# Optimization experiments

Measured on AMD Instinct MI355X. Metric: run time of the kernel, lower is better.

## Reference

```python
import jax, jax.numpy as jnp
import numpy as np

E = 64          # num experts
IN = 512        # input_size
OUT = 512       # output_size
N = 131072      # total tokens = sum(expert_size)
CAP = 3072      # static per-expert capacity (>= max expert_size)


def _make_expert_sizes():
    # uneven but deterministic sizes summing to N, all <= CAP
    rng = np.random.default_rng(0)
    sizes = np.full(E, N // E, dtype=np.int32)
    d = rng.integers(0, 513, size=E // 2).astype(np.int32)
    sizes[0::2] += d
    sizes[1::2] -= d
    assert sizes.sum() == N and sizes.max() <= CAP and sizes.min() > 0
    return jnp.asarray(sizes, dtype=jnp.int32)


def setup_inputs() -> dict:
    key = jax.random.key(0)
    k1, k2 = jax.random.split(key)
    inputs = jax.random.normal(k1, (N, IN), dtype=jnp.float32)
    # matches nn.init.uniform_(weight, -1/in, 1/in)
    weight = jax.random.uniform(k2, (E, IN, OUT), dtype=jnp.float32,
                                minval=-1.0 / IN, maxval=1.0 / IN)
    expert_size = _make_expert_sizes()
    return {"inputs": inputs, "expert_size": expert_size, "weight": weight}


def reference(inputs, expert_size, weight):
    # Grouped GEMM: tokens are pre-sorted by expert; segment e is
    # inputs[offset[e]:offset[e]+expert_size[e]] @ weight[e].
    cap_ids = jnp.arange(CAP, dtype=jnp.int32)                # [CAP]
    offsets = jnp.cumsum(expert_size) - expert_size           # [E]
    idx = offsets[:, None] + cap_ids[None, :]                 # [E, CAP]
    valid = cap_ids[None, :] < expert_size[:, None]           # [E, CAP]
    idx = jnp.where(valid, idx, N)                            # invalid -> OOB (dropped)
    # gather tokens into padded per-expert blocks; invalid slots -> 0
    x = jnp.take(inputs, idx, axis=0, mode='fill', fill_value=0.0)  # [E, CAP, IN]
    h = jnp.einsum('eci,eio->eco', x, weight)                 # [E, CAP, OUT]
    out = jnp.zeros((N, OUT), dtype=inputs.dtype)
    out = out.at[idx.reshape(-1)].add(h.reshape(-1, OUT), mode='drop')
    return out
```

## Files before the change

### kernel.cpp

```cpp
#include <hip/hip_runtime.h>
#include <hip/hip_bf16.h>

#define E_NUM 64
#define IN_SZ 512
#define OUT_SZ 512
#define N_TOK 131072
#define CAP 3072

#define BM 256
#define BN 256
#define BK 64
#define THREADS 512
#define RT_MAX 12
#define CT_NUM 2
#define JT 8
#define NWG (E_NUM * RT_MAX * CT_NUM)

typedef __attribute__((ext_vector_type(8))) short short8;
typedef __attribute__((ext_vector_type(4))) float f32x4;

__device__ inline unsigned short f2bf(float f) {
    unsigned int u = __float_as_uint(f);
    unsigned int r = (u + 0x7FFF + ((u >> 16) & 1)) >> 16;
    return (unsigned short)r;
}

__device__ inline unsigned int cvtpk(float a, float b) {
    unsigned int r;
    asm("v_cvt_pk_bf16_f32 %0, %1, %2" : "=v"(r) : "v"(a), "v"(b));
    return r;
}

#define GLOAD_LDS16(g, l)                                                     \
    __builtin_amdgcn_global_load_lds(                                         \
        (const __attribute__((address_space(1))) void*)(g),                   \
        (__attribute__((address_space(3))) void*)(l), 16, 0, 0)

__global__ void offsets_kernel(const int* __restrict__ sizes, int* __restrict__ offs) {
    int e = threadIdx.x;
    int s = 0;
    for (int i = 0; i < e; ++i) s += sizes[i];
    offs[e] = s;
}

__global__ __launch_bounds__(256) void prep_wt(const float* __restrict__ W,
                                               unsigned short* __restrict__ WT) {
    __shared__ float t[32][33];
    int k0 = blockIdx.x * 32, n0 = blockIdx.y * 32, e = blockIdx.z;
    const float* We = W + (size_t)e * IN_SZ * OUT_SZ;
    int tid = threadIdx.x;
    int r = tid >> 3, c4 = (tid & 7) * 4;
    float4 v = *(const float4*)(We + (size_t)(k0 + r) * OUT_SZ + n0 + c4);
    t[r][c4 + 0] = v.x; t[r][c4 + 1] = v.y; t[r][c4 + 2] = v.z; t[r][c4 + 3] = v.w;
    __syncthreads();
    ushort4 o;
    o.x = f2bf(t[c4 + 0][r]);
    o.y = f2bf(t[c4 + 1][r]);
    o.z = f2bf(t[c4 + 2][r]);
    o.w = f2bf(t[c4 + 3][r]);
    unsigned short* O = WT + (size_t)e * IN_SZ * OUT_SZ + (size_t)(n0 + r) * IN_SZ + k0 + c4;
    *(ushort4*)O = o;
}

__global__ __launch_bounds__(THREADS, 2) void gemm_moe(
    const float* __restrict__ A, const int* __restrict__ sizes,
    const unsigned short* __restrict__ WT, const int* __restrict__ offs,
    float* __restrict__ out)
{
    int b0 = blockIdx.x;
    int wg = (b0 & 7) * (NWG / 8) + (b0 >> 3);
    int ct = wg & (CT_NUM - 1);
    int rt = (wg >> 1) % RT_MAX;
    int e  = wg / (RT_MAX * CT_NUM);

    int size_e = sizes[e];
    int rows0 = rt * BM;
    if (rows0 >= size_e) return;
    int off_e = offs[e];
    int rows_rem = size_e - rows0;
    int maxr = (rows_rem < BM ? rows_rem : BM) - 1;

    __shared__ unsigned short lsA[2][BM * BK];
    __shared__ unsigned short lsB[2][BN * BK];

    int tid = threadIdx.x, l = tid & 63, w = tid >> 6;
    const char* WTe = (const char*)(WT + (size_t)e * IN_SZ * OUT_SZ);
    const float* Abase = A + (size_t)(off_e + rows0) * IN_SZ;

    int aoff[4];
    #pragma unroll
    for (int jj = 0; jj < 4; ++jj) {
        int u = tid + THREADS * jj;
        int row = u >> 3, s = u & 7;
        int c = s ^ (row & 7);
        int gr = row <= maxr ? row : maxr;
        aoff[jj] = gr * IN_SZ + c * 8;
    }
    int boff[4];
    #pragma unroll
    for (int i = 0; i < 4; ++i) {
        int unit = (w * 4 + i) * 64 + l;
        int row = unit >> 3, s = unit & 7;
        int c = s ^ (row & 7);
        boff[i] = (ct * BN + row) * (IN_SZ * 2) + c * 16;
    }

    f32x4 ar[8];

    auto loadA = [&](int kt) {
        #pragma unroll
        for (int jj = 0; jj < 4; ++jj) {
            ar[2 * jj]     = *(const f32x4*)(Abase + aoff[jj] + kt * BK);
            ar[2 * jj + 1] = *(const f32x4*)(Abase + aoff[jj] + kt * BK + 4);
        }
    };
    auto writeA = [&](int buf) {
        #pragma unroll
        for (int jj = 0; jj < 4; ++jj) {
            unsigned int p0 = cvtpk(ar[2 * jj][0], ar[2 * jj][1]);
            unsigned int p1 = cvtpk(ar[2 * jj][2], ar[2 * jj][3]);
            unsigned int p2 = cvtpk(ar[2 * jj + 1][0], ar[2 * jj + 1][1]);
            unsigned int p3 = cvtpk(ar[2 * jj + 1][2], ar[2 * jj + 1][3]);
            uint4 pk = make_uint4(p0, p1, p2, p3);
            *(uint4*)((char*)&lsA[buf][0] + (tid + THREADS * jj) * 16) = pk;
        }
    };
    auto stageB = [&](int buf, int kt) {
        #pragma unroll
        for (int i = 0; i < 4; ++i)
            GLOAD_LDS16(WTe + boff[i] + kt * 128, &lsB[buf][(w * 4 + i) * 512]);
    };

    int wm = (w >> 2) * 128, wn = (w & 3) * 64;
    int lrow = l & 15, kq = l >> 4;
    int abm[8], bbn[4];
    #pragma unroll
    for (int mm = 0; mm < 8; ++mm) abm[mm] = (wm + mm * 16 + lrow) * 128;
    #pragma unroll
    for (int nn = 0; nn < 4; ++nn) bbn[nn] = (wn + nn * 16 + lrow) * 128;
    int sk0 = ((0 * 4 + kq) ^ (lrow & 7)) * 16;
    int sk1 = ((1 * 4 + kq) ^ (lrow & 7)) * 16;

    f32x4 acc[8][4] = {};

    loadA(0); stageB(0, 0);
    writeA(0);
    __syncthreads();

    #pragma unroll
    for (int j = 0; j < JT; ++j) {
        int cur = j & 1;
        if (j + 1 < JT) {
            loadA(j + 1);
            stageB(cur ^ 1, j + 1);
        }
        {
            const char* pA = (const char*)&lsA[cur][0];
            const char* pB = (const char*)&lsB[cur][0];
            __builtin_amdgcn_s_setprio(1);
            #pragma unroll
            for (int ks = 0; ks < 2; ++ks) {
                int sk = ks ? sk1 : sk0;
                short8 bfr[4];
                #pragma unroll
                for (int nn = 0; nn < 4; ++nn)
                    bfr[nn] = *(const short8*)(pB + bbn[nn] + sk);
                #pragma unroll
                for (int mm = 0; mm < 8; ++mm) {
                    short8 af = *(const short8*)(pA + abm[mm] + sk);
                    #pragma unroll
                    for (int nn = 0; nn < 4; ++nn)
                        acc[mm][nn] = __builtin_amdgcn_mfma_f32_16x16x32_bf16(
                            af, bfr[nn], acc[mm][nn], 0, 0, 0);
                }
            }
            __builtin_amdgcn_s_setprio(0);
        }
        if (j + 1 < JT)
            writeA(cur ^ 1);
        if (j < JT - 1)
            __syncthreads();
    }

    float* outb = out + (size_t)(off_e + rows0) * OUT_SZ + ct * BN + wn;
    #pragma unroll
    for (int mm = 0; mm < 8; ++mm) {
        #pragma unroll
        for (int jj = 0; jj < 4; ++jj) {
            int rl = wm + mm * 16 + kq * 4 + jj;
            if (rl < rows_rem) {
                float* po = outb + (size_t)rl * OUT_SZ + lrow;
                #pragma unroll
                for (int nn = 0; nn < 4; ++nn)
                    po[nn * 16] = acc[mm][nn][jj];
            }
        }
    }
}

extern "C" void kernel_launch(void* const* d_in, const int* in_sizes, int n_in,
                              void* d_out, int out_size, void* d_ws, size_t ws_size,
                              hipStream_t stream) {
    const float* A      = (const float*)d_in[0];
    const int* sizes    = (const int*)d_in[1];
    const float* W      = (const float*)d_in[2];
    float* out          = (float*)d_out;

    unsigned short* WT  = (unsigned short*)d_ws;
    int* offs           = (int*)((char*)d_ws + (size_t)E_NUM * IN_SZ * OUT_SZ * 2);

    offsets_kernel<<<1, E_NUM, 0, stream>>>(sizes, offs);
    prep_wt<<<dim3(IN_SZ / 32, OUT_SZ / 32, E_NUM), 256, 0, stream>>>(W, WT);
    gemm_moe<<<NWG, THREADS, 0, stream>>>(A, sizes, WT, offs, out);
}
```

Measured before the change: 184.5 us.

## Triple-buffer B tiles and interleave split prefetches with MFMA phases

Triples the B shared-memory buffer so that weight tiles are prefetched two k-steps ahead. Each k-step is split into four MFMA phases, with half-sized A/B prefetches and LDS reads placed between workgroup barriers. Full __syncthreads is replaced by manual vmcnt/lgkmcnt waits plus s_barrier, so global loads overlap the matrix math more finely. In exchange it adds many barriers per iteration and raises shared memory to 160KB. It also depends on fragile hand-counted vmcnt values that must match the ordering of the A and B loads.

```diff
diff --git a/kernel.cpp b/kernel.cpp
--- a/kernel.cpp
+++ b/kernel.cpp
@@ -81,7 +81,7 @@
     int maxr = (rows_rem < BM ? rows_rem : BM) - 1;
 
     __shared__ unsigned short lsA[2][BM * BK];
-    __shared__ unsigned short lsB[2][BN * BK];
+    __shared__ unsigned short lsB[3][BN * BK];
 
     int tid = threadIdx.x, l = tid & 63, w = tid >> 6;
     const char* WTe = (const char*)(WT + (size_t)e * IN_SZ * OUT_SZ);
@@ -107,9 +107,9 @@
 
     f32x4 ar[8];
 
-    auto loadA = [&](int kt) {
-        #pragma unroll
-        for (int jj = 0; jj < 4; ++jj) {
+    auto loadA_h = [&](int kt, int h) {
+        #pragma unroll
+        for (int jj = 2 * h; jj < 2 * h + 2; ++jj) {
             ar[2 * jj]     = *(const f32x4*)(Abase + aoff[jj] + kt * BK);
             ar[2 * jj + 1] = *(const f32x4*)(Abase + aoff[jj] + kt * BK + 4);
         }
@@ -125,9 +125,9 @@
             *(uint4*)((char*)&lsA[buf][0] + (tid + THREADS * jj) * 16) = pk;
         }
     };
-    auto stageB = [&](int buf, int kt) {
-        #pragma unroll
-        for (int i = 0; i < 4; ++i)
+    auto stageB_h = [&](int buf, int kt, int h) {
+        #pragma unroll
+        for (int i = 2 * h; i < 2 * h + 2; ++i)
             GLOAD_LDS16(WTe + boff[i] + kt * 128, &lsB[buf][(w * 4 + i) * 512]);
     };
 
@@ -143,43 +143,76 @@
 
     f32x4 acc[8][4] = {};
 
-    loadA(0); stageB(0, 0);
+    #define RD_A(mh, sk)                                                      \
+        _Pragma("unroll")                                                     \
+        for (int i = 0; i < 4; ++i)                                           \
+            af[i] = *(const short8*)(pA + abm[(mh) * 4 + i] + (sk));
+    #define RD_B(sk)                                                          \
+        _Pragma("unroll")                                                     \
+        for (int n = 0; n < 4; ++n)                                           \
+            bfr[n] = *(const short8*)(pB + bbn[n] + (sk));
+    #define MFMA16(mh)                                                        \
+        __builtin_amdgcn_s_setprio(1);                                        \
+        _Pragma("unroll")                                                     \
+        for (int i = 0; i < 4; ++i)                                           \
+            _Pragma("unroll")                                                 \
+            for (int n = 0; n < 4; ++n)                                       \
+                acc[(mh) * 4 + i][n] = __builtin_amdgcn_mfma_f32_16x16x32_bf16(\
+                    af[i], bfr[n], acc[(mh) * 4 + i][n], 0, 0, 0);            \
+        __builtin_amdgcn_s_setprio(0);
+
+    loadA_h(0, 0); loadA_h(0, 1);
+    stageB_h(0, 0, 0); stageB_h(0, 0, 1);
+    stageB_h(1, 1, 0); stageB_h(1, 1, 1);
     writeA(0);
-    __syncthreads();
-
-    #pragma unroll
-    for (int j = 0; j < JT; ++j) {
-        int cur = j & 1;
-        if (j + 1 < JT) {
-            loadA(j + 1);
-            stageB(cur ^ 1, j + 1);
-        }
-        {
-            const char* pA = (const char*)&lsA[cur][0];
-            const char* pB = (const char*)&lsB[cur][0];
-            __builtin_amdgcn_s_setprio(1);
-            #pragma unroll
-            for (int ks = 0; ks < 2; ++ks) {
-                int sk = ks ? sk1 : sk0;
-                short8 bfr[4];
-                #pragma unroll
-                for (int nn = 0; nn < 4; ++nn)
-                    bfr[nn] = *(const short8*)(pB + bbn[nn] + sk);
-                #pragma unroll
-                for (int mm = 0; mm < 8; ++mm) {
-                    short8 af = *(const short8*)(pA + abm[mm] + sk);
-                    #pragma unroll
-                    for (int nn = 0; nn < 4; ++nn)
-                        acc[mm][nn] = __builtin_amdgcn_mfma_f32_16x16x32_bf16(
-                            af, bfr[nn], acc[mm][nn], 0, 0, 0);
-                }
+    asm volatile("s_waitcnt vmcnt(4)" ::: "memory");
+    __builtin_amdgcn_sched_barrier(0);
+    asm volatile("s_waitcnt lgkmcnt(0)" ::: "memory");
+    __builtin_amdgcn_sched_barrier(0);
+    __builtin_amdgcn_s_barrier();
+    __builtin_amdgcn_sched_barrier(0);
+
+    #pragma unroll
+    for (int t = 0; t < JT; ++t) {
+        const char* pA = (const char*)&lsA[t & 1][0];
+        const char* pB = (const char*)&lsB[t % 3][0];
+        short8 af[4], bfr[4];
+
+        RD_A(0, sk0); RD_B(sk0);
+        if (t + 1 < JT) loadA_h(t + 1, 0);
+        __builtin_amdgcn_s_barrier();
+        MFMA16(0);
+        __builtin_amdgcn_s_barrier();
+
+        RD_A(1, sk0);
+        if (t + 1 < JT) loadA_h(t + 1, 1);
+        __builtin_amdgcn_s_barrier();
+        MFMA16(1);
+        __builtin_amdgcn_s_barrier();
+
+        RD_A(0, sk1); RD_B(sk1);
+        if (t + 2 < JT) stageB_h((t + 2) % 3, t + 2, 0);
+        __builtin_amdgcn_s_barrier();
+        MFMA16(0);
+        __builtin_amdgcn_s_barrier();
+
+        RD_A(1, sk1);
+        if (t + 2 < JT) stageB_h((t + 2) % 3, t + 2, 1);
+        if (t + 1 < JT) writeA((t + 1) & 1);
+        __builtin_amdgcn_s_barrier();
+        MFMA16(1);
+        if (t < JT - 1) {
+            if (t + 2 < JT) {
+                asm volatile("s_waitcnt vmcnt(4)" ::: "memory");
+            } else {
+                asm volatile("s_waitcnt vmcnt(0)" ::: "memory");
             }
-            __builtin_amdgcn_s_setprio(0);
-        }
-        if (j + 1 < JT)
-            writeA(cur ^ 1);
-        if (j < JT - 1)
-            __syncthreads();
+            __builtin_amdgcn_sched_barrier(0);
+            asm volatile("s_waitcnt lgkmcnt(0)" ::: "memory");
+            __builtin_amdgcn_sched_barrier(0);
+            __builtin_amdgcn_s_barrier();
+            __builtin_amdgcn_sched_barrier(0);
+        }
     }
 
     float* outb = out + (size_t)(off_e + rows0) * OUT_SZ + ct * BN + wn;
```

New measurement: 221.9 us. +20.3%, slower.
